# Performance work log

Hardware: AMD Instinct MI355X
Metric: run time of the kernel (lower is better)

The kernel has to match this reference:

```python
import jax, jax.numpy as jnp
import numpy as np

VIEW_R = 32
SCALING = 16.0 / 8.0  # lora_alpha / r


def setup_inputs() -> dict:
    key = jax.random.key(0)
    ks = jax.random.split(key, 12)
    bs, S, d, r = 64, 256, 768, 8
    n = d // VIEW_R  # 24
    return {
        "x": jax.random.normal(ks[0], (bs, S, d), jnp.float32),
        "user_h": jax.random.normal(ks[1], (bs, d), jnp.float32),
        "item_h": jax.random.normal(ks[2], (bs, d), jnp.float32),
        "W": jax.random.normal(ks[3], (d, d), jnp.float32) * 0.02,   # base weight (out,in)
        "b": jax.random.normal(ks[4], (d,), jnp.float32) * 0.02,
        "A": jax.random.normal(ks[5], (r, d), jnp.float32) * 0.02,   # lora_A
        "B": jax.random.normal(ks[6], (d, r), jnp.float32) * 0.02,   # lora_B (zeros at init; randomized to exercise math)
        "Wu": jax.random.normal(ks[7], (d, d), jnp.float32) * 0.02,  # lora_U weight (out,in)
        "VU": jax.random.normal(ks[8], (n, VIEW_R), jnp.float32) * 0.02,
        "Wi": jax.random.normal(ks[9], (d, d), jnp.float32) * 0.02,  # lora_I weight
        "VI": jax.random.normal(ks[10], (n, VIEW_R), jnp.float32) * 0.02,
    }


def _kron_branch(x, h, Wlin, V):
    # original: weight[b, q*n_in + n, l*32 + m] = (h @ Wlin.T)[b, q, l] * V[n, m]
    #           result[b,s,:] = x[b,s,:] @ weight[b]
    # factorized form (same math, no (bs, d, d) intermediate):
    bs, S, d = x.shape
    n, m = V.shape
    q = VIEW_R
    l = d // VIEW_R
    wq = (h @ Wlin.T).reshape(bs, q, l)          # (b, q, l)
    x4 = x.reshape(bs, S, q, n)                  # d split as (q, n)
    t = jnp.einsum("bsqn,nm->bsqm", x4, V)
    out = jnp.einsum("bsqm,bql->bslm", t, wq)    # out index = l*32 + m
    return out.reshape(bs, S, d)


def reference(x, user_h, item_h, W, b, A, B, Wu, VU, Wi, VI):
    # F.linear + LoRA
    out = jnp.einsum("bsd,od->bso", x, W) + b
    out = out + jnp.einsum("bsd,rd,or->bso", x, A, B) * SCALING
    # user Kronecker low-rank per-sample weight branch
    out = out + _kron_branch(x, user_h, Wu, VU)
    # item branch
    out = out + _kron_branch(x, item_h, Wi, VI)
    return out
```

## Files before the change

kernel.cpp:

```cpp
#include <hip/hip_runtime.h>
#include <hip/hip_bf16.h>

typedef __bf16 bf16x8 __attribute__((ext_vector_type(8)));
typedef float f32x4 __attribute__((ext_vector_type(4)));
typedef unsigned short u16x8 __attribute__((ext_vector_type(8)));

__device__ __forceinline__ unsigned short f2bf(float f) {
    unsigned int u = __builtin_bit_cast(unsigned int, f);
    unsigned int r = (u + 0x7FFFu + ((u >> 16) & 1u)) >> 16;
    return (unsigned short)r;
}

__device__ __forceinline__ void load_lds_16(const void* g, void* lds) {
    __builtin_amdgcn_global_load_lds(
        (const __attribute__((address_space(1))) unsigned int*)g,
        (__attribute__((address_space(3))) unsigned int*)lds, 16, 0, 0);
}

__global__ __launch_bounds__(256) void prep_kernel(
    const float* __restrict__ x, unsigned short* __restrict__ xb,
    const float* __restrict__ W, const float* __restrict__ A,
    const float* __restrict__ B, unsigned short* __restrict__ weffB,
    const float* __restrict__ uh, const float* __restrict__ ih,
    const float* __restrict__ Wu, const float* __restrict__ Wi,
    float* __restrict__ wqu_p, float* __restrict__ wqi_p) {
    __shared__ __align__(16) float Wl[64 * 100];
    __shared__ __align__(16) float Hl[32 * 100];
    const int bx = blockIdx.x;
    const int t = threadIdx.x;
    if (bx < 384) {
        const int g = bx % 24, j = bx / 24;
        const int br = g / 12, ot = g % 12;
        const int bt = j & 1, ks = j >> 1;
        const int o0 = ot * 64, b0 = bt * 32, k0 = ks * 96;
        const float* h = (br ? ih : uh);
        const float* Wm = (br ? Wi : Wu);
        for (int i = t; i < 1536; i += 256) {
            int row = i / 24, c = i % 24;
            *(float4*)&Wl[row * 100 + c * 4] =
                *(const float4*)(Wm + (size_t)(o0 + row) * 768 + k0 + c * 4);
        }
        for (int i = t; i < 768; i += 256) {
            int row = i / 24, c = i % 24;
            *(float4*)&Hl[row * 100 + c * 4] =
                *(const float4*)(h + (size_t)(b0 + row) * 768 + k0 + c * 4);
        }
        __syncthreads();
        const int o2 = t & 31, b4 = t >> 5;
        float acc[2][4] = {};
#pragma unroll 6
        for (int k4 = 0; k4 < 24; ++k4) {
            float4 w0 = *(const float4*)&Wl[o2 * 100 + k4 * 4];
            float4 w1 = *(const float4*)&Wl[(o2 + 32) * 100 + k4 * 4];
#pragma unroll
            for (int jj = 0; jj < 4; ++jj) {
                float4 hb = *(const float4*)&Hl[(b4 * 4 + jj) * 100 + k4 * 4];
                acc[0][jj] += w0.x * hb.x + w0.y * hb.y + w0.z * hb.z + w0.w * hb.w;
                acc[1][jj] += w1.x * hb.x + w1.y * hb.y + w1.z * hb.z + w1.w * hb.w;
            }
        }
        float* part = (br ? wqi_p : wqu_p) + (size_t)ks * 49152;
#pragma unroll
        for (int oo = 0; oo < 2; ++oo)
#pragma unroll
            for (int jj = 0; jj < 4; ++jj)
                part[(size_t)(b0 + b4 * 4 + jj) * 768 + o0 + o2 + oo * 32] = acc[oo][jj];
    } else if (bx < 2688) {
        int idx = bx - 384;
        int o = idx / 3;
        int k = (idx % 3) * 256 + t;
        float acc = W[o * 768 + k];
#pragma unroll
        for (int r = 0; r < 8; ++r) acc += 2.0f * B[o * 8 + r] * A[r * 768 + k];
        weffB[o * 768 + k] = f2bf(acc);
    } else {
        int b2 = bx - 2688;
        const float4* xp = (const float4*)x;
        float4 a[4], c[4];
        int i0 = b2 * 1024 + t;
#pragma unroll
        for (int u = 0; u < 4; ++u) {
            int i = i0 + u * 256;
            a[u] = xp[i * 2];
            c[u] = xp[i * 2 + 1];
        }
#pragma unroll
        for (int u = 0; u < 4; ++u) {
            int i = i0 + u * 256;
            u16x8 r;
            r[0] = f2bf(a[u].x); r[1] = f2bf(a[u].y); r[2] = f2bf(a[u].z); r[3] = f2bf(a[u].w);
            r[4] = f2bf(c[u].x); r[5] = f2bf(c[u].y); r[6] = f2bf(c[u].z); r[7] = f2bf(c[u].w);
            *(u16x8*)(xb + (size_t)i * 8) = r;
        }
    }
}

__global__ __launch_bounds__(256, 3) void gemm_fused_kernel(
    const unsigned short* __restrict__ Xb, const unsigned short* __restrict__ WeffB,
    const float* __restrict__ VU, const float* __restrict__ VI,
    const float* __restrict__ wqu_p, const float* __restrict__ wqi_p,
    const float* __restrict__ bias, float* __restrict__ out) {
    __shared__ __align__(16) unsigned short As[128 * 64];
    __shared__ __align__(16) unsigned short Bs[128 * 64];
    __shared__ __align__(16) unsigned int vui[32 * 26];
    __shared__ __align__(16) float wqs[32 * 8];
    __shared__ float bias_s[128];
    const int tid = threadIdx.x;
    const int wave = tid >> 6, lane = tid & 63;
    const int id = blockIdx.x;
    const int nt = id >> 7, rem = id & 127, b = rem >> 1, mt = rem & 1;
    const int s0 = mt * 128, n0 = nt * 128;

    for (int i = tid; i < 768; i += 256) {
        int n = i >> 5, m = i & 31;
        vui[m * 26 + n] = ((unsigned int)f2bf(VU[i]) << 16) | (unsigned int)f2bf(VI[i]);
    }
    {
        int q = tid >> 3, g = (tid >> 1) & 3, brs = tid & 1;
        const float* p = (brs ? wqi_p : wqu_p) + b * 768 + q * 24 + nt * 4 + g;
        float s = 0.0f;
#pragma unroll
        for (int ks = 0; ks < 8; ++ks) s += p[(size_t)ks * 49152];
        wqs[tid] = s;
    }
    if (tid < 128) bias_s[tid] = bias[n0 + tid];
    __syncthreads();

    const unsigned short* Abase = Xb + (size_t)(b * 256 + s0) * 768;
    const unsigned short* Bbase = WeffB + (size_t)n0 * 768;
    const int wm = wave & 1, wn = wave >> 1;
    const int lrow = lane >> 3, lcp = lane & 7;
    const int rg = tid >> 3, cc = tid & 7;
    const int sl = cc ^ (rg & 7);
    const unsigned short* Wp0 = Bbase + (size_t)rg * 768 + cc * 8;

    f32x4 acc[4][4] = {};
    u16x8 wreg[4];
#pragma unroll
    for (int g = 0; g < 4; ++g) wreg[g] = *(const u16x8*)(Wp0 + (size_t)g * 32 * 768);

    for (int kk = 0; kk < 768; kk += 64) {
#pragma unroll
        for (int u = 0; u < 4; ++u) {
            int tA = wave * 4 + u;
            int r = tA * 8 + lrow;
            int c = lcp ^ (r & 7);
            load_lds_16(Abase + (size_t)r * 768 + kk + c * 8, (void*)(As + tA * 512));
        }
        {
            int kb = kk + cc * 8;
            int q = (kb * 2731) >> 16;
            int n0c = kb - q * 24;
            const unsigned int* vp = &vui[rg * 26 + n0c];
            uint2 pv01 = *(const uint2*)(vp);
            uint2 pv23 = *(const uint2*)(vp + 2);
            uint2 pv45 = *(const uint2*)(vp + 4);
            uint2 pv67 = *(const uint2*)(vp + 6);
            unsigned int pv[8] = {pv01.x, pv01.y, pv23.x, pv23.y, pv45.x, pv45.y, pv67.x, pv67.y};
            float fu[8], fi[8];
#pragma unroll
            for (int j = 0; j < 8; ++j) {
                fu[j] = __builtin_bit_cast(float, pv[j] & 0xFFFF0000u);
                fi[j] = __builtin_bit_cast(float, pv[j] << 16);
            }
            const float4* wp4 = (const float4*)&wqs[q * 8];
            float4 wa = wp4[0], wb = wp4[1];
            float wu[4] = {wa.x, wa.z, wb.x, wb.z};
            float wi[4] = {wa.y, wa.w, wb.y, wb.w};
#pragma unroll
            for (int g = 0; g < 4; ++g) {
                uint4 wd = __builtin_bit_cast(uint4, wreg[g]);
                unsigned int warr[4] = {wd.x, wd.y, wd.z, wd.w};
                unsigned int kvw[4];
#pragma unroll
                for (int p = 0; p < 4; ++p) {
                    float lo = __builtin_bit_cast(float, warr[p] << 16);
                    float hi = __builtin_bit_cast(float, warr[p] & 0xFFFF0000u);
                    float v0 = fmaf(fi[2 * p],     wi[g], fmaf(fu[2 * p],     wu[g], lo));
                    float v1 = fmaf(fi[2 * p + 1], wi[g], fmaf(fu[2 * p + 1], wu[g], hi));
                    kvw[p] = __builtin_amdgcn_perm(__builtin_bit_cast(unsigned int, v1),
                                                   __builtin_bit_cast(unsigned int, v0),
                                                   0x07060302u);
                }
                *(uint4*)(Bs + (g * 32 + rg) * 64 + sl * 8) =
                    make_uint4(kvw[0], kvw[1], kvw[2], kvw[3]);
            }
        }
        __syncthreads();
        if (kk < 704) {
            const unsigned short* Wn = Wp0 + kk + 64;
#pragma unroll
            for (int g = 0; g < 4; ++g) wreg[g] = *(const u16x8*)(Wn + (size_t)g * 32 * 768);
        }
#pragma unroll
        for (int h = 0; h < 2; ++h) {
            const int cb = h * 4 + (lane >> 4);
            const int rl = lane & 15;
            bf16x8 af[4], bw[4];
#pragma unroll
            for (int i = 0; i < 4; ++i) {
                int r = wm * 64 + i * 16 + rl;
                int c = cb ^ (r & 7);
                af[i] = *(const bf16x8*)(As + r * 64 + c * 8);
            }
#pragma unroll
            for (int j = 0; j < 4; ++j) {
                int r = wn * 64 + j * 16 + rl;
                int c = cb ^ (r & 7);
                bw[j] = *(const bf16x8*)(Bs + r * 64 + c * 8);
            }
#pragma unroll
            for (int i = 0; i < 4; ++i)
#pragma unroll
                for (int j = 0; j < 4; ++j)
                    acc[i][j] = __builtin_amdgcn_mfma_f32_16x16x32_bf16(af[i], bw[j], acc[i][j], 0, 0, 0);
        }
        __syncthreads();
    }

    const int cl = lane & 15, rq = lane >> 4;
#pragma unroll
    for (int j = 0; j < 4; ++j) {
        int nn = wn * 64 + j * 16 + cl;
        float bv = bias_s[nn];
#pragma unroll
        for (int i = 0; i < 4; ++i) {
            int mrow = s0 + wm * 64 + i * 16 + rq * 4;
            float* op = out + (size_t)(b * 256 + mrow) * 768 + n0 + nn;
#pragma unroll
            for (int g = 0; g < 4; ++g) op[(size_t)g * 768] = acc[i][j][g] + bv;
        }
    }
}

__global__ void weff_kernel(const float* __restrict__ W, const float* __restrict__ A,
                            const float* __restrict__ B, float* __restrict__ Weff) {
    int o = blockIdx.x / 3;
    int k = (blockIdx.x % 3) * 256 + threadIdx.x;
    float acc = W[o * 768 + k];
#pragma unroll
    for (int r = 0; r < 8; ++r) acc += 2.0f * B[o * 8 + r] * A[r * 768 + k];
    Weff[o * 768 + k] = acc;
}

__global__ void wq2_kernel(const float* __restrict__ uh, const float* __restrict__ ih,
                           const float* __restrict__ Wu, const float* __restrict__ Wi,
                           float* __restrict__ wqu, float* __restrict__ wqi) {
    int bx = blockIdx.x;
    int og = bx % 192;
    int rest = bx / 192;
    int b = rest & 63;
    int br = rest >> 6;
    int wave = threadIdx.x >> 6, lane = threadIdx.x & 63;
    int o = og * 4 + wave;
    const float* h = (br ? ih : uh) + b * 768;
    const float* Wrow = (br ? Wi : Wu) + (size_t)o * 768;
    const float4* hp = (const float4*)(h + lane * 12);
    const float4* wp = (const float4*)(Wrow + lane * 12);
    float s = 0.0f;
#pragma unroll
    for (int j = 0; j < 3; ++j) {
        float4 hv = hp[j], wv = wp[j];
        s += hv.x * wv.x + hv.y * wv.y + hv.z * wv.z + hv.w * wv.w;
    }
#pragma unroll
    for (int off = 32; off; off >>= 1) s += __shfl_down(s, off);
    if (lane == 0) (br ? wqi : wqu)[b * 768 + o] = s;
}

__global__ void naive_kernel(const float* __restrict__ x, const float* __restrict__ Weff,
                             const float* __restrict__ wqu, const float* __restrict__ wqi,
                             const float* __restrict__ VU, const float* __restrict__ VI,
                             const float* __restrict__ bias, float* __restrict__ out) {
    int bs_ = blockIdx.x / 3;
    int chunk = blockIdx.x % 3;
    int b = bs_ >> 8;
    __shared__ float xs[768];
    for (int i = threadIdx.x; i < 768; i += 256) xs[i] = x[(size_t)bs_ * 768 + i];
    __syncthreads();
    int o = chunk * 256 + threadIdx.x;
    int m = o & 31, l = o >> 5;
    float acc = bias[o];
    for (int q = 0; q < 32; ++q) {
        float wu = wqu[b * 768 + q * 24 + l];
        float wi = wqi[b * 768 + q * 24 + l];
#pragma unroll
        for (int n = 0; n < 24; ++n) {
            int k = q * 24 + n;
            float w = Weff[o * 768 + k] + VU[n * 32 + m] * wu + VI[n * 32 + m] * wi;
            acc += xs[k] * w;
        }
    }
    out[(size_t)bs_ * 768 + o] = acc;
}

extern "C" void kernel_launch(void* const* d_in, const int* in_sizes, int n_in,
                              void* d_out, int out_size, void* d_ws, size_t ws_size,
                              hipStream_t stream) {
    const float* x  = (const float*)d_in[0];
    const float* uh = (const float*)d_in[1];
    const float* ih = (const float*)d_in[2];
    const float* W  = (const float*)d_in[3];
    const float* bv = (const float*)d_in[4];
    const float* A  = (const float*)d_in[5];
    const float* B  = (const float*)d_in[6];
    const float* Wu = (const float*)d_in[7];
    const float* VU = (const float*)d_in[8];
    const float* Wi = (const float*)d_in[9];
    const float* VI = (const float*)d_in[10];
    float* out = (float*)d_out;

    const size_t off_xb   = 0;
    const size_t off_weff = 25165824;
    const size_t off_wqu  = off_weff + 1179648;
    const size_t off_wqi  = off_wqu + 1572864;
    const size_t need     = off_wqi + 1572864;

    char* ws = (char*)d_ws;
    if (ws_size >= need) {
        unsigned short* xb    = (unsigned short*)(ws + off_xb);
        unsigned short* weffB = (unsigned short*)(ws + off_weff);
        float* wqu_p = (float*)(ws + off_wqu);
        float* wqi_p = (float*)(ws + off_wqi);
        prep_kernel<<<4224, 256, 0, stream>>>(x, xb, W, A, B, weffB, uh, ih, Wu, Wi, wqu_p, wqi_p);
        gemm_fused_kernel<<<768, 256, 0, stream>>>(xb, weffB, VU, VI, wqu_p, wqi_p, bv, out);
    } else {
        float* weff = (float*)ws;
        float* wqu  = weff + 589824;
        float* wqi  = wqu + 49152;
        weff_kernel<<<2304, 256, 0, stream>>>(W, A, B, weff);
        wq2_kernel<<<24576, 256, 0, stream>>>(uh, ih, Wu, Wi, wqu, wqi);
        naive_kernel<<<49152, 256, 0, stream>>>(x, weff, wqu, wqi, VU, VI, bv, out);
    }
}
```

Before: 148.8 us.

## Double-buffer LDS tiles with BK=32 to overlap loads and B-build with MFMA

Splits the K loop into 32-wide steps with two LDS buffers for A and the fused B tile. The next step's async A loads and on-the-fly B construction are issued before the current step's MFMAs, which removes one barrier per iteration and hides global-load latency. The thread mapping for building B and the LDS swizzle are changed to fit the 32-column tiles. The cost is twice as many loop iterations and barriers over K, and the smaller MFMA batch per barrier may limit overlap.

New measurement: 153.4 us. 1.03x slower.

```diff
diff --git a/kernel.cpp b/kernel.cpp
--- a/kernel.cpp
+++ b/kernel.cpp
@@ -100,8 +100,8 @@
     const float* __restrict__ VU, const float* __restrict__ VI,
     const float* __restrict__ wqu_p, const float* __restrict__ wqi_p,
     const float* __restrict__ bias, float* __restrict__ out) {
-    __shared__ __align__(16) unsigned short As[128 * 64];
-    __shared__ __align__(16) unsigned short Bs[128 * 64];
+    __shared__ __align__(16) unsigned short As[2][128 * 32];
+    __shared__ __align__(16) unsigned short Bs[2][128 * 32];
     __shared__ __align__(16) unsigned int vui[32 * 26];
     __shared__ __align__(16) float wqs[32 * 8];
     __shared__ float bias_s[128];
@@ -129,92 +129,105 @@
     const unsigned short* Abase = Xb + (size_t)(b * 256 + s0) * 768;
     const unsigned short* Bbase = WeffB + (size_t)n0 * 768;
     const int wm = wave & 1, wn = wave >> 1;
-    const int lrow = lane >> 3, lcp = lane & 7;
-    const int rg = tid >> 3, cc = tid & 7;
-    const int sl = cc ^ (rg & 7);
+    const int rg = tid >> 2, cc = tid & 3;
+    const int sl = cc ^ ((rg >> 1) & 3);
+    const int m_i = rg & 31, lg0 = rg >> 5;
     const unsigned short* Wp0 = Bbase + (size_t)rg * 768 + cc * 8;
 
     f32x4 acc[4][4] = {};
-    u16x8 wreg[4];
-#pragma unroll
-    for (int g = 0; g < 4; ++g) wreg[g] = *(const u16x8*)(Wp0 + (size_t)g * 32 * 768);
-
-    for (int kk = 0; kk < 768; kk += 64) {
-#pragma unroll
-        for (int u = 0; u < 4; ++u) {
-            int tA = wave * 4 + u;
-            int r = tA * 8 + lrow;
-            int c = lcp ^ (r & 7);
-            load_lds_16(Abase + (size_t)r * 768 + kk + c * 8, (void*)(As + tA * 512));
-        }
-        {
-            int kb = kk + cc * 8;
-            int q = (kb * 2731) >> 16;
-            int n0c = kb - q * 24;
-            const unsigned int* vp = &vui[rg * 26 + n0c];
-            uint2 pv01 = *(const uint2*)(vp);
-            uint2 pv23 = *(const uint2*)(vp + 2);
-            uint2 pv45 = *(const uint2*)(vp + 4);
-            uint2 pv67 = *(const uint2*)(vp + 6);
-            unsigned int pv[8] = {pv01.x, pv01.y, pv23.x, pv23.y, pv45.x, pv45.y, pv67.x, pv67.y};
-            float fu[8], fi[8];
-#pragma unroll
-            for (int j = 0; j < 8; ++j) {
-                fu[j] = __builtin_bit_cast(float, pv[j] & 0xFFFF0000u);
-                fi[j] = __builtin_bit_cast(float, pv[j] << 16);
+    u16x8 wreg[2];
+
+    auto ldreg = [&](int kk) {
+#pragma unroll
+        for (int g = 0; g < 2; ++g)
+            wreg[g] = *(const u16x8*)(Wp0 + (size_t)g * 64 * 768 + kk);
+    };
+
+    auto build = [&](int kkb, unsigned short* bs_w) {
+        int kb = kkb + cc * 8;
+        int q = (kb * 2731) >> 16;
+        int n0c = kb - q * 24;
+        const unsigned int* vp = &vui[m_i * 26 + n0c];
+        uint2 pv01 = *(const uint2*)(vp);
+        uint2 pv23 = *(const uint2*)(vp + 2);
+        uint2 pv45 = *(const uint2*)(vp + 4);
+        uint2 pv67 = *(const uint2*)(vp + 6);
+        unsigned int pv[8] = {pv01.x, pv01.y, pv23.x, pv23.y, pv45.x, pv45.y, pv67.x, pv67.y};
+        float fu[8], fi[8];
+#pragma unroll
+        for (int j = 0; j < 8; ++j) {
+            fu[j] = __builtin_bit_cast(float, pv[j] & 0xFFFF0000u);
+            fi[j] = __builtin_bit_cast(float, pv[j] << 16);
+        }
+        const float4* wp4 = (const float4*)&wqs[q * 8];
+        float4 wa = wp4[0], wb = wp4[1];
+        float wu_[2] = {lg0 ? wa.z : wa.x, lg0 ? wb.z : wb.x};
+        float wi_[2] = {lg0 ? wa.w : wa.y, lg0 ? wb.w : wb.y};
+#pragma unroll
+        for (int g = 0; g < 2; ++g) {
+            float wu = wu_[g], wi = wi_[g];
+            uint4 wd = __builtin_bit_cast(uint4, wreg[g]);
+            unsigned int warr[4] = {wd.x, wd.y, wd.z, wd.w};
+            unsigned int kvw[4];
+#pragma unroll
+            for (int p = 0; p < 4; ++p) {
+                float lo = __builtin_bit_cast(float, warr[p] << 16);
+                float hi = __builtin_bit_cast(float, warr[p] & 0xFFFF0000u);
+                float v0 = fmaf(fi[2 * p],     wi, fmaf(fu[2 * p],     wu, lo));
+                float v1 = fmaf(fi[2 * p + 1], wi, fmaf(fu[2 * p + 1], wu, hi));
+                kvw[p] = __builtin_amdgcn_perm(__builtin_bit_cast(unsigned int, v1),
+                                               __builtin_bit_cast(unsigned int, v0),
+                                               0x07060302u);
             }
-            const float4* wp4 = (const float4*)&wqs[q * 8];
-            float4 wa = wp4[0], wb = wp4[1];
-            float wu[4] = {wa.x, wa.z, wb.x, wb.z};
-            float wi[4] = {wa.y, wa.w, wb.y, wb.w};
-#pragma unroll
-            for (int g = 0; g < 4; ++g) {
-                uint4 wd = __builtin_bit_cast(uint4, wreg[g]);
-                unsigned int warr[4] = {wd.x, wd.y, wd.z, wd.w};
-                unsigned int kvw[4];
-#pragma unroll
-                for (int p = 0; p < 4; ++p) {
-                    float lo = __builtin_bit_cast(float, warr[p] << 16);
-                    float hi = __builtin_bit_cast(float, warr[p] & 0xFFFF0000u);
-                    float v0 = fmaf(fi[2 * p],     wi[g], fmaf(fu[2 * p],     wu[g], lo));
-                    float v1 = fmaf(fi[2 * p + 1], wi[g], fmaf(fu[2 * p + 1], wu[g], hi));
-                    kvw[p] = __builtin_amdgcn_perm(__builtin_bit_cast(unsigned int, v1),
-                                                   __builtin_bit_cast(unsigned int, v0),
-                                                   0x07060302u);
-                }
-                *(uint4*)(Bs + (g * 32 + rg) * 64 + sl * 8) =
-                    make_uint4(kvw[0], kvw[1], kvw[2], kvw[3]);
-            }
-        }
-        __syncthreads();
-        if (kk < 704) {
-            const unsigned short* Wn = Wp0 + kk + 64;
-#pragma unroll
-            for (int g = 0; g < 4; ++g) wreg[g] = *(const u16x8*)(Wn + (size_t)g * 32 * 768);
-        }
-#pragma unroll
-        for (int h = 0; h < 2; ++h) {
-            const int cb = h * 4 + (lane >> 4);
-            const int rl = lane & 15;
-            bf16x8 af[4], bw[4];
-#pragma unroll
-            for (int i = 0; i < 4; ++i) {
-                int r = wm * 64 + i * 16 + rl;
-                int c = cb ^ (r & 7);
-                af[i] = *(const bf16x8*)(As + r * 64 + c * 8);
-            }
-#pragma unroll
-            for (int j = 0; j < 4; ++j) {
-                int r = wn * 64 + j * 16 + rl;
-                int c = cb ^ (r & 7);
-                bw[j] = *(const bf16x8*)(Bs + r * 64 + c * 8);
-            }
-#pragma unroll
-            for (int i = 0; i < 4; ++i)
-#pragma unroll
-                for (int j = 0; j < 4; ++j)
-                    acc[i][j] = __builtin_amdgcn_mfma_f32_16x16x32_bf16(af[i], bw[j], acc[i][j], 0, 0, 0);
-        }
+            *(uint4*)(bs_w + (g * 64 + rg) * 32 + sl * 8) =
+                make_uint4(kvw[0], kvw[1], kvw[2], kvw[3]);
+        }
+    };
+
+    auto dma_A = [&](int kk, unsigned short* as_w) {
+#pragma unroll
+        for (int d = 0; d < 2; ++d) {
+            int r = (wave * 2 + d) * 16 + (lane >> 2);
+            int c = (lane & 3) ^ ((r >> 1) & 3);
+            load_lds_16(Abase + (size_t)r * 768 + kk + c * 8,
+                        (void*)(as_w + (wave * 2 + d) * 512));
+        }
+    };
+
+    dma_A(0, &As[0][0]);
+    ldreg(0);
+    build(0, &Bs[0][0]);
+    ldreg(32);
+    __syncthreads();
+
+    for (int t = 0; t < 24; ++t) {
+        const int kk = t * 32;
+        if (t < 23) {
+            dma_A(kk + 32, &As[(t + 1) & 1][0]);
+            build(kk + 32, &Bs[(t + 1) & 1][0]);
+            if (t < 22) ldreg(kk + 64);
+        }
+        const unsigned short* as_r = &As[t & 1][0];
+        const unsigned short* bs_r = &Bs[t & 1][0];
+        const int cb = lane >> 4, rl = lane & 15;
+        bf16x8 af[4], bw[4];
+#pragma unroll
+        for (int i = 0; i < 4; ++i) {
+            int r = wm * 64 + i * 16 + rl;
+            int c = cb ^ ((r >> 1) & 3);
+            af[i] = *(const bf16x8*)(as_r + r * 32 + c * 8);
+        }
+#pragma unroll
+        for (int j = 0; j < 4; ++j) {
+            int r = wn * 64 + j * 16 + rl;
+            int c = cb ^ ((r >> 1) & 3);
+            bw[j] = *(const bf16x8*)(bs_r + r * 32 + c * 8);
+        }
+#pragma unroll
+        for (int i = 0; i < 4; ++i)
+#pragma unroll
+            for (int j = 0; j < 4; ++j)
+                acc[i][j] = __builtin_amdgcn_mfma_f32_16x16x32_bf16(af[i], bw[j], acc[i][j], 0, 0, 0);
         __syncthreads();
     }
 
```
